# Performance work log

Measured on AMD Instinct MI355X. Metric: run time of the kernel, lower is better.

Reference implementation:

```python
import jax, jax.numpy as jnp
import numpy as np


def setup_inputs() -> dict:
    key = jax.random.key(0)
    kq, kk, kv = jax.random.split(key, 3)
    B, S, D = 16, 2048, 128
    q = jax.random.normal(kq, (B, S, D), dtype=jnp.float32)
    k = jax.random.normal(kk, (B, S, D), dtype=jnp.float32)
    v = jax.random.normal(kv, (B, S, D), dtype=jnp.float32)
    return {"q": q, "k": k, "v": v}


def reference(q, k, v):
    # q: (B, Sq, Dk), k: (B, Skv, Dk), v: (B, Skv, Dv)
    d_k = k.shape[-1]
    scale = 1.0 / jnp.sqrt(jnp.asarray(d_k, dtype=q.dtype))
    scores = jnp.einsum("bqd,bkd->bqk", q, k) * scale  # (B, Sq, Skv)
    # causal mask: strictly-upper-triangular positions set to -inf (mask=True in init)
    Sq = q.shape[-2]
    causal = jnp.triu(jnp.ones((Sq, Sq), dtype=bool), k=1)
    scores = jnp.where(causal, -jnp.inf, scores)
    attn = jax.nn.softmax(scores, axis=-1)
    return jnp.einsum("bqk,bkd->bqd", attn, v)
```

## Files before the change

kernel.cpp:

```cpp
#include <hip/hip_runtime.h>
#include <hip/hip_bf16.h>

typedef __bf16 bf16;
typedef bf16 bf16x8 __attribute__((ext_vector_type(8)));
typedef bf16 bf16x4 __attribute__((ext_vector_type(4)));
typedef float f32x4 __attribute__((ext_vector_type(4)));

#define DHEAD 128
#define SCL2 0.1275500811965365f
#define NINF (-__builtin_inff())

__device__ __forceinline__ unsigned pk2(float a, float b) {
  bf16 x = (bf16)a, y = (bf16)b;
  unsigned short ux = __builtin_bit_cast(unsigned short, x);
  unsigned short uy = __builtin_bit_cast(unsigned short, y);
  return ((unsigned)uy << 16) | (unsigned)ux;
}

#define ACC_FLOATS (1024 * 64 * 128)
#define ML_OFF ACC_FLOATS
#define WS_NEED ((size_t)(ACC_FLOATS + 1024 * 64 * 2) * 4)

__global__ __launch_bounds__(256) void fa_split(
    const float* __restrict__ Q, const float* __restrict__ K,
    const float* __restrict__ V, float* __restrict__ ws, int S)
{
  const int bid  = blockIdx.x;
  const int r    = bid >> 8;
  const int i    = bid & 255;
  const int b    = i & 15;
  const int idx  = i >> 4;
  const int qt   = (r < 2) ? (31 - idx) : idx;
  const int half = r & 1;
  const int blk  = bid;

  const int t0 = half * (qt + 1);
  const int t1 = t0 + (qt + 1);

  const int tid  = threadIdx.x;
  const int wave = tid >> 6;
  const int lane = tid & 63;
  const int lr   = lane & 15;
  const int lg   = lane >> 4;

  __shared__ bf16 Ks[2][32][136];
  __shared__ bf16 Vt[2][DHEAD][40];
  __shared__ bf16 Ps[4][16][40];

  const size_t bo = (size_t)b * S * DHEAD;
  const float* Qb = Q + bo + (size_t)qt * 64 * DHEAD;
  const float* Kb = K + bo;
  const float* Vb = V + bo;
  const int wrow0 = qt * 64 + wave * 16;

  const int j   = tid & 31;
  const int prw = tid >> 5;
  const int d4  = j << 2;
  const int Gw  = (j >> 1) & 3;

  bf16x8 qf[4];
  {
    const float* qr = Qb + (size_t)(wave * 16 + lr) * DHEAD;
    #pragma unroll
    for (int c = 0; c < 4; ++c) {
      const float4 u0 = *reinterpret_cast<const float4*>(qr + c * 32 + lg * 8);
      const float4 u1 = *reinterpret_cast<const float4*>(qr + c * 32 + lg * 8 + 4);
      bf16x8 f;
      f[0] = (bf16)u0.x; f[1] = (bf16)u0.y; f[2] = (bf16)u0.z; f[3] = (bf16)u0.w;
      f[4] = (bf16)u1.x; f[5] = (bf16)u1.y; f[6] = (bf16)u1.z; f[7] = (bf16)u1.w;
      qf[c] = f;
    }
  }

  f32x4 oacc[8];
  #pragma unroll
  for (int ii = 0; ii < 8; ++ii) oacc[ii] = (f32x4){0.f, 0.f, 0.f, 0.f};
  float m = NINF, l = 0.f;

  float4 kA[2], kB[2], vA[2], vB[2];
  auto load_tile = [&](int kc) {
    #pragma unroll
    for (int ps = 0; ps < 2; ++ps) {
      const int kv = kc + 2 * (prw + 8 * ps);
      const float* kp = Kb + (size_t)kv * DHEAD + d4;
      const float* vp = Vb + (size_t)kv * DHEAD + d4;
      kA[ps] = *reinterpret_cast<const float4*>(kp);
      kB[ps] = *reinterpret_cast<const float4*>(kp + DHEAD);
      vA[ps] = *reinterpret_cast<const float4*>(vp);
      vB[ps] = *reinterpret_cast<const float4*>(vp + DHEAD);
    }
  };
  auto write_tile = [&](int buf) {
    #pragma unroll
    for (int ps = 0; ps < 2; ++ps) {
      const int kvp = prw + 8 * ps;
      bf16x4 ka, kb;
      ka[0] = (bf16)kA[ps].x; ka[1] = (bf16)kA[ps].y;
      ka[2] = (bf16)kA[ps].z; ka[3] = (bf16)kA[ps].w;
      kb[0] = (bf16)kB[ps].x; kb[1] = (bf16)kB[ps].y;
      kb[2] = (bf16)kB[ps].z; kb[3] = (bf16)kB[ps].w;
      *reinterpret_cast<bf16x4*>(&Ks[buf][2 * kvp][d4])     = ka;
      *reinterpret_cast<bf16x4*>(&Ks[buf][2 * kvp + 1][d4]) = kb;
      const int pS = kvp ^ (Gw << 2);
      const float* fa = &vA[ps].x;
      const float* fb = &vB[ps].x;
      #pragma unroll
      for (int c = 0; c < 4; ++c) {
        *reinterpret_cast<unsigned*>(&Vt[buf][d4 + c][2 * pS]) = pk2(fa[c], fb[c]);
      }
    }
  };

  load_tile(t0 * 32);
  write_tile(0);
  if (t0 + 1 < t1) load_tile((t0 + 1) * 32);

  int cur = 0;
  for (int t = t0; t < t1; ++t) {
    __syncthreads();
    if (t + 1 < t1) write_tile(cur ^ 1);
    if (t + 2 < t1) load_tile((t + 2) * 32);

    const int kc = t * 32;
    if (kc <= wrow0 + 15) {
      f32x4 s0 = {0.f, 0.f, 0.f, 0.f}, s1 = {0.f, 0.f, 0.f, 0.f};
      __builtin_amdgcn_s_setprio(1);
      #pragma unroll
      for (int c = 0; c < 4; ++c) {
        const bf16x8 kf0 = *reinterpret_cast<const bf16x8*>(&Ks[cur][lr][c * 32 + lg * 8]);
        const bf16x8 kf1 = *reinterpret_cast<const bf16x8*>(&Ks[cur][16 + lr][c * 32 + lg * 8]);
        s0 = __builtin_amdgcn_mfma_f32_16x16x32_bf16(kf0, qf[c], s0, 0, 0, 0);
        s1 = __builtin_amdgcn_mfma_f32_16x16x32_bf16(kf1, qf[c], s1, 0, 0, 0);
      }
      __builtin_amdgcn_s_setprio(0);

      const int qg = wrow0 + lr;
      float x0[4], x1[4];
      if (kc + 31 > wrow0) {
        #pragma unroll
        for (int rr = 0; rr < 4; ++rr) {
          x0[rr] = (kc + 4 * lg + rr      > qg) ? NINF : s0[rr] * SCL2;
          x1[rr] = (kc + 16 + 4 * lg + rr > qg) ? NINF : s1[rr] * SCL2;
        }
      } else {
        #pragma unroll
        for (int rr = 0; rr < 4; ++rr) { x0[rr] = s0[rr] * SCL2; x1[rr] = s1[rr] * SCL2; }
      }
      float tm = NINF;
      #pragma unroll
      for (int rr = 0; rr < 4; ++rr) tm = fmaxf(tm, fmaxf(x0[rr], x1[rr]));
      tm = fmaxf(tm, __shfl_xor(tm, 16));
      tm = fmaxf(tm, __shfl_xor(tm, 32));

      if (!__all(tm <= m + 8.0f)) {
        const float mn = fmaxf(m, tm);
        const float al = __builtin_exp2f(m - mn);
        m = mn; l *= al;
        #pragma unroll
        for (int rr = 0; rr < 4; ++rr) {
          const float ar = __shfl(al, 4 * lg + rr);
          #pragma unroll
          for (int ds = 0; ds < 8; ++ds) oacc[ds][rr] *= ar;
        }
      }

      float p0[4], p1[4];
      float ts = 0.f;
      #pragma unroll
      for (int rr = 0; rr < 4; ++rr) {
        p0[rr] = __builtin_exp2f(x0[rr] - m);
        p1[rr] = __builtin_exp2f(x1[rr] - m);
        ts += p0[rr] + p1[rr];
      }
      ts += __shfl_xor(ts, 16);
      ts += __shfl_xor(ts, 32);
      l += ts;

      *reinterpret_cast<unsigned*>(&Ps[wave][lr][4 * lg])          = pk2(p0[0], p0[1]);
      *reinterpret_cast<unsigned*>(&Ps[wave][lr][4 * lg + 2])      = pk2(p0[2], p0[3]);
      *reinterpret_cast<unsigned*>(&Ps[wave][lr][16 + 4 * lg])     = pk2(p1[0], p1[1]);
      *reinterpret_cast<unsigned*>(&Ps[wave][lr][16 + 4 * lg + 2]) = pk2(p1[2], p1[3]);

      const bf16x8 pf = *reinterpret_cast<const bf16x8*>(&Ps[wave][lr][lg * 8]);
      __builtin_amdgcn_s_setprio(1);
      #pragma unroll
      for (int ds = 0; ds < 8; ++ds) {
        const int G = (2 * ds + (lr >> 3)) & 3;
        const bf16x8 vf = *reinterpret_cast<const bf16x8*>(&Vt[cur][ds * 16 + lr][8 * (lg ^ G)]);
        oacc[ds] = __builtin_amdgcn_mfma_f32_16x16x32_bf16(pf, vf, oacc[ds], 0, 0, 0);
      }
      __builtin_amdgcn_s_setprio(0);
    }
    cur ^= 1;
  }

  float* aw = ws + (size_t)blk * 8192 + (size_t)(wave * 16) * 128;
  #pragma unroll
  for (int rr = 0; rr < 4; ++rr) {
    #pragma unroll
    for (int ds = 0; ds < 8; ++ds) {
      aw[(4 * lg + rr) * 128 + ds * 16 + lr] = oacc[ds][rr];
    }
  }
  if (lg == 0) {
    float* mlp = ws + ML_OFF + (size_t)(blk * 64 + wave * 16 + lr) * 2;
    mlp[0] = m;
    mlp[1] = l;
  }
}

__global__ __launch_bounds__(256) void fa_merge(
    const float* __restrict__ ws, float* __restrict__ O, int S)
{
  const int blk2 = blockIdx.x;
  const int b  = blk2 >> 5;
  const int qt = blk2 & 31;
  const int tid = threadIdx.x;
  const int row = tid >> 2;
  const int c0  = (tid & 3) * 32;

  const int idx  = (qt >= 16) ? (31 - qt) : qt;
  const int base = (qt >= 16) ? 0 : 512;
  const int blk0 = base + (idx << 4) + b;
  const int blk1 = blk0 + 256;

  const float* ml0 = ws + ML_OFF + (size_t)(blk0 * 64 + row) * 2;
  const float* ml1 = ws + ML_OFF + (size_t)(blk1 * 64 + row) * 2;
  const float m0 = ml0[0], l0 = ml0[1];
  const float m1 = ml1[0], l1 = ml1[1];
  const float mm = fmaxf(m0, m1);
  const float a0 = __builtin_exp2f(m0 - mm);
  const float a1 = __builtin_exp2f(m1 - mm);
  const float inv = 1.0f / (a0 * l0 + a1 * l1);

  const float* w0 = ws + (size_t)blk0 * 8192 + (size_t)row * 128 + c0;
  const float* w1 = ws + (size_t)blk1 * 8192 + (size_t)row * 128 + c0;
  float* out = O + ((size_t)b * S + qt * 64 + row) * DHEAD + c0;

  #pragma unroll
  for (int qd = 0; qd < 8; ++qd) {
    const float4 u0 = *reinterpret_cast<const float4*>(w0 + qd * 4);
    const float4 u1 = *reinterpret_cast<const float4*>(w1 + qd * 4);
    float4 o;
    o.x = (a0 * u0.x + a1 * u1.x) * inv;
    o.y = (a0 * u0.y + a1 * u1.y) * inv;
    o.z = (a0 * u0.z + a1 * u1.z) * inv;
    o.w = (a0 * u0.w + a1 * u1.w) * inv;
    *reinterpret_cast<float4*>(out + qd * 4) = o;
  }
}

__global__ __launch_bounds__(256) void fa_fwd(
    const float* __restrict__ Q, const float* __restrict__ K,
    const float* __restrict__ V, float* __restrict__ O, int S)
{
  const int bid = blockIdx.x;
  const int prb = bid & 255;
  const int hb  = bid >> 8;
  const int b   = prb & 15;
  const int jj  = prb >> 4;
  const int qt  = hb ? jj : (31 - jj);

  const int tid  = threadIdx.x;
  const int wave = tid >> 6;
  const int lane = tid & 63;
  const int lr   = lane & 15;
  const int lg   = lane >> 4;

  __shared__ bf16 Ks[2][32][136];
  __shared__ bf16 Vt[2][DHEAD][40];
  __shared__ bf16 Ps[4][16][40];

  const size_t bo = (size_t)b * S * DHEAD;
  const float* Qb = Q + bo + (size_t)qt * 64 * DHEAD;
  const float* Kb = K + bo;
  const float* Vb = V + bo;
  const int wrow0 = qt * 64 + wave * 16;

  const int j   = tid & 31;
  const int prw = tid >> 5;
  const int d4  = j << 2;
  const int Gw  = (j >> 1) & 3;

  bf16x8 qf[4];
  {
    const float* qr = Qb + (size_t)(wave * 16 + lr) * DHEAD;
    #pragma unroll
    for (int c = 0; c < 4; ++c) {
      const float4 u0 = *reinterpret_cast<const float4*>(qr + c * 32 + lg * 8);
      const float4 u1 = *reinterpret_cast<const float4*>(qr + c * 32 + lg * 8 + 4);
      bf16x8 f;
      f[0] = (bf16)u0.x; f[1] = (bf16)u0.y; f[2] = (bf16)u0.z; f[3] = (bf16)u0.w;
      f[4] = (bf16)u1.x; f[5] = (bf16)u1.y; f[6] = (bf16)u1.z; f[7] = (bf16)u1.w;
      qf[c] = f;
    }
  }

  f32x4 oacc[8];
  #pragma unroll
  for (int ii = 0; ii < 8; ++ii) oacc[ii] = (f32x4){0.f, 0.f, 0.f, 0.f};
  float m = NINF, l = 0.f;

  const int nt = 2 * (qt + 1);
  float4 kA[2], kB[2], vA[2], vB[2];

  auto load_tile = [&](int kc) {
    #pragma unroll
    for (int ps = 0; ps < 2; ++ps) {
      const int kv = kc + 2 * (prw + 8 * ps);
      const float* kp = Kb + (size_t)kv * DHEAD + d4;
      const float* vp = Vb + (size_t)kv * DHEAD + d4;
      kA[ps] = *reinterpret_cast<const float4*>(kp);
      kB[ps] = *reinterpret_cast<const float4*>(kp + DHEAD);
      vA[ps] = *reinterpret_cast<const float4*>(vp);
      vB[ps] = *reinterpret_cast<const float4*>(vp + DHEAD);
    }
  };
  auto write_tile = [&](int buf) {
    #pragma unroll
    for (int ps = 0; ps < 2; ++ps) {
      const int kvp = prw + 8 * ps;
      bf16x4 ka, kb;
      ka[0] = (bf16)kA[ps].x; ka[1] = (bf16)kA[ps].y;
      ka[2] = (bf16)kA[ps].z; ka[3] = (bf16)kA[ps].w;
      kb[0] = (bf16)kB[ps].x; kb[1] = (bf16)kB[ps].y;
      kb[2] = (bf16)kB[ps].z; kb[3] = (bf16)kB[ps].w;
      *reinterpret_cast<bf16x4*>(&Ks[buf][2 * kvp][d4])     = ka;
      *reinterpret_cast<bf16x4*>(&Ks[buf][2 * kvp + 1][d4]) = kb;
      const int pS = kvp ^ (Gw << 2);
      const float* fa = &vA[ps].x;
      const float* fb = &vB[ps].x;
      #pragma unroll
      for (int c = 0; c < 4; ++c) {
        *reinterpret_cast<unsigned*>(&Vt[buf][d4 + c][2 * pS]) = pk2(fa[c], fb[c]);
      }
    }
  };

  load_tile(0);
  write_tile(0);
  if (nt > 1) load_tile(32);

  int cur = 0;
  for (int t = 0; t < nt; ++t) {
    __syncthreads();
    if (t + 1 < nt) write_tile(cur ^ 1);
    if (t + 2 < nt) load_tile((t + 2) * 32);

    const int kc = t * 32;
    if (kc <= wrow0 + 15) {
      f32x4 s0 = {0.f, 0.f, 0.f, 0.f}, s1 = {0.f, 0.f, 0.f, 0.f};
      __builtin_amdgcn_s_setprio(1);
      #pragma unroll
      for (int c = 0; c < 4; ++c) {
        const bf16x8 kf0 = *reinterpret_cast<const bf16x8*>(&Ks[cur][lr][c * 32 + lg * 8]);
        const bf16x8 kf1 = *reinterpret_cast<const bf16x8*>(&Ks[cur][16 + lr][c * 32 + lg * 8]);
        s0 = __builtin_amdgcn_mfma_f32_16x16x32_bf16(kf0, qf[c], s0, 0, 0, 0);
        s1 = __builtin_amdgcn_mfma_f32_16x16x32_bf16(kf1, qf[c], s1, 0, 0, 0);
      }
      __builtin_amdgcn_s_setprio(0);

      const int qg = wrow0 + lr;
      float x0[4], x1[4];
      if (kc + 31 > wrow0) {
        #pragma unroll
        for (int rr = 0; rr < 4; ++rr) {
          x0[rr] = (kc + 4 * lg + rr      > qg) ? NINF : s0[rr] * SCL2;
          x1[rr] = (kc + 16 + 4 * lg + rr > qg) ? NINF : s1[rr] * SCL2;
        }
      } else {
        #pragma unroll
        for (int rr = 0; rr < 4; ++rr) { x0[rr] = s0[rr] * SCL2; x1[rr] = s1[rr] * SCL2; }
      }
      float tm = NINF;
      #pragma unroll
      for (int rr = 0; rr < 4; ++rr) tm = fmaxf(tm, fmaxf(x0[rr], x1[rr]));
      tm = fmaxf(tm, __shfl_xor(tm, 16));
      tm = fmaxf(tm, __shfl_xor(tm, 32));

      if (!__all(tm <= m + 8.0f)) {
        const float mn = fmaxf(m, tm);
        const float al = __builtin_exp2f(m - mn);
        m = mn; l *= al;
        #pragma unroll
        for (int rr = 0; rr < 4; ++rr) {
          const float ar = __shfl(al, 4 * lg + rr);
          #pragma unroll
          for (int ds = 0; ds < 8; ++ds) oacc[ds][rr] *= ar;
        }
      }

      float p0[4], p1[4];
      float ts = 0.f;
      #pragma unroll
      for (int rr = 0; rr < 4; ++rr) {
        p0[rr] = __builtin_exp2f(x0[rr] - m);
        p1[rr] = __builtin_exp2f(x1[rr] - m);
        ts += p0[rr] + p1[rr];
      }
      ts += __shfl_xor(ts, 16);
      ts += __shfl_xor(ts, 32);
      l += ts;

      *reinterpret_cast<unsigned*>(&Ps[wave][lr][4 * lg])          = pk2(p0[0], p0[1]);
      *reinterpret_cast<unsigned*>(&Ps[wave][lr][4 * lg + 2])      = pk2(p0[2], p0[3]);
      *reinterpret_cast<unsigned*>(&Ps[wave][lr][16 + 4 * lg])     = pk2(p1[0], p1[1]);
      *reinterpret_cast<unsigned*>(&Ps[wave][lr][16 + 4 * lg + 2]) = pk2(p1[2], p1[3]);

      const bf16x8 pf = *reinterpret_cast<const bf16x8*>(&Ps[wave][lr][lg * 8]);
      __builtin_amdgcn_s_setprio(1);
      #pragma unroll
      for (int ds = 0; ds < 8; ++ds) {
        const int G = (2 * ds + (lr >> 3)) & 3;
        const bf16x8 vf = *reinterpret_cast<const bf16x8*>(&Vt[cur][ds * 16 + lr][8 * (lg ^ G)]);
        oacc[ds] = __builtin_amdgcn_mfma_f32_16x16x32_bf16(pf, vf, oacc[ds], 0, 0, 0);
      }
      __builtin_amdgcn_s_setprio(0);
    }
    cur ^= 1;
  }

  const float linv = 1.0f / l;
  float* Ob = O + bo + (size_t)(qt * 64 + wave * 16) * DHEAD;
  #pragma unroll
  for (int rr = 0; rr < 4; ++rr) {
    const float ir = __shfl(linv, 4 * lg + rr);
    #pragma unroll
    for (int ds = 0; ds < 8; ++ds) {
      Ob[(size_t)(4 * lg + rr) * DHEAD + ds * 16 + lr] = oacc[ds][rr] * ir;
    }
  }
}

extern "C" void kernel_launch(void* const* d_in, const int* in_sizes, int n_in,
                              void* d_out, int out_size, void* d_ws, size_t ws_size,
                              hipStream_t stream) {
  const float* q = (const float*)d_in[0];
  const float* k = (const float*)d_in[1];
  const float* v = (const float*)d_in[2];
  float* o = (float*)d_out;

  const int B = 16;
  const int S = in_sizes[0] / (B * DHEAD);

  if (ws_size >= WS_NEED && S == 2048) {
    float* ws = (float*)d_ws;
    fa_split<<<dim3(1024), dim3(256), 0, stream>>>(q, k, v, ws, S);
    fa_merge<<<dim3(512), dim3(256), 0, stream>>>(ws, o, S);
  } else {
    fa_fwd<<<dim3(512), dim3(256), 0, stream>>>(q, k, v, o, S);
  }
}
```

Measured before the change: 161.1 us.

## Split causal attention KV range four ways per query tile with merge kernel

Adds a four-way split-KV flash attention path. Every query tile's causal key range is divided into four equal chunks, and each chunk runs in its own block (2048 blocks), replacing the earlier two-way split that paired tiles for balance. A merge kernel then combines the four partials using their saved max and sum values. The aim is more parallelism and better load balance across the GPU's compute units, at the cost of twice the workspace traffic for partial outputs plus extra merge work.

```diff
diff --git a/kernel.cpp b/kernel.cpp
--- a/kernel.cpp
+++ b/kernel.cpp
@@ -20,6 +20,237 @@
 #define ACC_FLOATS (1024 * 64 * 128)
 #define ML_OFF ACC_FLOATS
 #define WS_NEED ((size_t)(ACC_FLOATS + 1024 * 64 * 2) * 4)
+
+#define ACC4_FLOATS (2048 * 64 * 128)
+#define ML4_OFF ACC4_FLOATS
+#define WS_NEED4 ((size_t)(ACC4_FLOATS + 2048 * 64 * 2) * 4)
+
+__global__ __launch_bounds__(256) void fa_split4(
+    const float* __restrict__ Q, const float* __restrict__ K,
+    const float* __restrict__ V, float* __restrict__ ws, int S)
+{
+  const int bid  = blockIdx.x;
+  const int half = bid >> 9;
+  const int w    = bid & 511;
+  const int qt   = 31 - (w >> 4);
+  const int b    = w & 15;
+  const int blk  = bid;
+
+  const int NT = 2 * (qt + 1);
+  const int t0 = (half * NT) >> 2;
+  const int t1 = ((half + 1) * NT) >> 2;
+
+  const int tid  = threadIdx.x;
+  const int wave = tid >> 6;
+  const int lane = tid & 63;
+  const int lr   = lane & 15;
+  const int lg   = lane >> 4;
+
+  __shared__ bf16 Ks[32][136];
+  __shared__ bf16 Vt[DHEAD][40];
+  __shared__ bf16 Ps[4][16][40];
+
+  const size_t bo = (size_t)b * S * DHEAD;
+  const float* Qb = Q + bo + (size_t)qt * 64 * DHEAD;
+  const float* Kb = K + bo;
+  const float* Vb = V + bo;
+  const int wrow0 = qt * 64 + wave * 16;
+
+  const int j   = tid & 31;
+  const int prw = tid >> 5;
+  const int d4  = j << 2;
+  const int Gw  = (j >> 1) & 3;
+
+  bf16x8 qf[4];
+  {
+    const float* qr = Qb + (size_t)(wave * 16 + lr) * DHEAD;
+    #pragma unroll
+    for (int c = 0; c < 4; ++c) {
+      const float4 u0 = *reinterpret_cast<const float4*>(qr + c * 32 + lg * 8);
+      const float4 u1 = *reinterpret_cast<const float4*>(qr + c * 32 + lg * 8 + 4);
+      bf16x8 f;
+      f[0] = (bf16)(u0.x * SCL2); f[1] = (bf16)(u0.y * SCL2);
+      f[2] = (bf16)(u0.z * SCL2); f[3] = (bf16)(u0.w * SCL2);
+      f[4] = (bf16)(u1.x * SCL2); f[5] = (bf16)(u1.y * SCL2);
+      f[6] = (bf16)(u1.z * SCL2); f[7] = (bf16)(u1.w * SCL2);
+      qf[c] = f;
+    }
+  }
+
+  f32x4 oacc[8];
+  #pragma unroll
+  for (int ii = 0; ii < 8; ++ii) oacc[ii] = (f32x4){0.f, 0.f, 0.f, 0.f};
+  float m = NINF, l = 0.f;
+
+  float4 kA[2], kB[2], vA[2], vB[2];
+  auto load_tile = [&](int kc) {
+    #pragma unroll
+    for (int ps = 0; ps < 2; ++ps) {
+      const int kv = kc + 2 * (prw + 8 * ps);
+      const float* kp = Kb + (size_t)kv * DHEAD + d4;
+      const float* vp = Vb + (size_t)kv * DHEAD + d4;
+      kA[ps] = *reinterpret_cast<const float4*>(kp);
+      kB[ps] = *reinterpret_cast<const float4*>(kp + DHEAD);
+      vA[ps] = *reinterpret_cast<const float4*>(vp);
+      vB[ps] = *reinterpret_cast<const float4*>(vp + DHEAD);
+    }
+  };
+  auto write_tile = [&]() {
+    #pragma unroll
+    for (int ps = 0; ps < 2; ++ps) {
+      const int kvp = prw + 8 * ps;
+      bf16x4 ka, kb;
+      ka[0] = (bf16)kA[ps].x; ka[1] = (bf16)kA[ps].y;
+      ka[2] = (bf16)kA[ps].z; ka[3] = (bf16)kA[ps].w;
+      kb[0] = (bf16)kB[ps].x; kb[1] = (bf16)kB[ps].y;
+      kb[2] = (bf16)kB[ps].z; kb[3] = (bf16)kB[ps].w;
+      *reinterpret_cast<bf16x4*>(&Ks[2 * kvp][d4])     = ka;
+      *reinterpret_cast<bf16x4*>(&Ks[2 * kvp + 1][d4]) = kb;
+      const int pS = kvp ^ (Gw << 2);
+      const float* fa = &vA[ps].x;
+      const float* fb = &vB[ps].x;
+      #pragma unroll
+      for (int c = 0; c < 4; ++c) {
+        *reinterpret_cast<unsigned*>(&Vt[d4 + c][2 * pS]) = pk2(fa[c], fb[c]);
+      }
+    }
+  };
+
+  if (t0 < t1) load_tile(t0 * 32);
+
+  for (int t = t0; t < t1; ++t) {
+    __syncthreads();
+    write_tile();
+    if (t + 1 < t1) load_tile((t + 1) * 32);
+    __syncthreads();
+
+    const int kc = t * 32;
+    if (kc <= wrow0 + 15) {
+      f32x4 s0 = {0.f, 0.f, 0.f, 0.f}, s1 = {0.f, 0.f, 0.f, 0.f};
+      __builtin_amdgcn_s_setprio(1);
+      #pragma unroll
+      for (int c = 0; c < 4; ++c) {
+        const bf16x8 kf0 = *reinterpret_cast<const bf16x8*>(&Ks[lr][c * 32 + lg * 8]);
+        const bf16x8 kf1 = *reinterpret_cast<const bf16x8*>(&Ks[16 + lr][c * 32 + lg * 8]);
+        s0 = __builtin_amdgcn_mfma_f32_16x16x32_bf16(kf0, qf[c], s0, 0, 0, 0);
+        s1 = __builtin_amdgcn_mfma_f32_16x16x32_bf16(kf1, qf[c], s1, 0, 0, 0);
+      }
+      __builtin_amdgcn_s_setprio(0);
+
+      const int qg = wrow0 + lr;
+      float x0[4], x1[4];
+      if (kc + 31 > wrow0) {
+        #pragma unroll
+        for (int rr = 0; rr < 4; ++rr) {
+          x0[rr] = (kc + 4 * lg + rr      > qg) ? NINF : s0[rr];
+          x1[rr] = (kc + 16 + 4 * lg + rr > qg) ? NINF : s1[rr];
+        }
+      } else {
+        #pragma unroll
+        for (int rr = 0; rr < 4; ++rr) { x0[rr] = s0[rr]; x1[rr] = s1[rr]; }
+      }
+      float tm = NINF;
+      #pragma unroll
+      for (int rr = 0; rr < 4; ++rr) tm = fmaxf(tm, fmaxf(x0[rr], x1[rr]));
+      tm = fmaxf(tm, __shfl_xor(tm, 16));
+      tm = fmaxf(tm, __shfl_xor(tm, 32));
+
+      if (!__all(tm <= m + 8.0f)) {
+        const float mn = fmaxf(m, tm);
+        const float al = __builtin_exp2f(m - mn);
+        m = mn; l *= al;
+        #pragma unroll
+        for (int rr = 0; rr < 4; ++rr) {
+          const float ar = __shfl(al, 4 * lg + rr);
+          #pragma unroll
+          for (int ds = 0; ds < 8; ++ds) oacc[ds][rr] *= ar;
+        }
+      }
+
+      float p0[4], p1[4];
+      float ts = 0.f;
+      #pragma unroll
+      for (int rr = 0; rr < 4; ++rr) {
+        p0[rr] = __builtin_exp2f(x0[rr] - m);
+        p1[rr] = __builtin_exp2f(x1[rr] - m);
+        ts += p0[rr] + p1[rr];
+      }
+      ts += __shfl_xor(ts, 16);
+      ts += __shfl_xor(ts, 32);
+      l += ts;
+
+      *reinterpret_cast<unsigned*>(&Ps[wave][lr][4 * lg])          = pk2(p0[0], p0[1]);
+      *reinterpret_cast<unsigned*>(&Ps[wave][lr][4 * lg + 2])      = pk2(p0[2], p0[3]);
+      *reinterpret_cast<unsigned*>(&Ps[wave][lr][16 + 4 * lg])     = pk2(p1[0], p1[1]);
+      *reinterpret_cast<unsigned*>(&Ps[wave][lr][16 + 4 * lg + 2]) = pk2(p1[2], p1[3]);
+
+      const bf16x8 pf = *reinterpret_cast<const bf16x8*>(&Ps[wave][lr][lg * 8]);
+      __builtin_amdgcn_s_setprio(1);
+      #pragma unroll
+      for (int ds = 0; ds < 8; ++ds) {
+        const int G = (2 * ds + (lr >> 3)) & 3;
+        const bf16x8 vf = *reinterpret_cast<const bf16x8*>(&Vt[ds * 16 + lr][8 * (lg ^ G)]);
+        oacc[ds] = __builtin_amdgcn_mfma_f32_16x16x32_bf16(pf, vf, oacc[ds], 0, 0, 0);
+      }
+      __builtin_amdgcn_s_setprio(0);
+    }
+  }
+
+  float* aw = ws + (size_t)blk * 8192 + (size_t)(wave * 16) * 128;
+  #pragma unroll
+  for (int rr = 0; rr < 4; ++rr) {
+    #pragma unroll
+    for (int ds = 0; ds < 8; ++ds) {
+      aw[(4 * lg + rr) * 128 + ds * 16 + lr] = oacc[ds][rr];
+    }
+  }
+  if (lg == 0) {
+    float* mlp = ws + ML4_OFF + (size_t)(blk * 64 + wave * 16 + lr) * 2;
+    mlp[0] = m;
+    mlp[1] = l;
+  }
+}
+
+__global__ __launch_bounds__(256) void fa_merge4(
+    const float* __restrict__ ws, float* __restrict__ O, int S)
+{
+  const int blk2 = blockIdx.x;
+  const int b  = blk2 >> 5;
+  const int qt = blk2 & 31;
+  const int tid = threadIdx.x;
+  const int row = tid >> 2;
+  const int c0  = (tid & 3) * 32;
+
+  const int w = (31 - qt) * 16 + b;
+  float mi[4], li[4];
+  float mm = NINF;
+  #pragma unroll
+  for (int i = 0; i < 4; ++i) {
+    const float* ml = ws + ML4_OFF + (size_t)((i * 512 + w) * 64 + row) * 2;
+    mi[i] = ml[0]; li[i] = ml[1];
+    mm = fmaxf(mm, mi[i]);
+  }
+  float a[4], den = 0.f;
+  #pragma unroll
+  for (int i = 0; i < 4; ++i) { a[i] = __builtin_exp2f(mi[i] - mm); den += a[i] * li[i]; }
+  const float inv = 1.0f / den;
+
+  float* out = O + ((size_t)b * S + qt * 64 + row) * DHEAD + c0;
+  #pragma unroll
+  for (int qd = 0; qd < 8; ++qd) {
+    float4 acc = {0.f, 0.f, 0.f, 0.f};
+    #pragma unroll
+    for (int i = 0; i < 4; ++i) {
+      const float* wp = ws + (size_t)(i * 512 + w) * 8192 + (size_t)row * 128 + c0;
+      const float4 u = *reinterpret_cast<const float4*>(wp + qd * 4);
+      acc.x += a[i] * u.x; acc.y += a[i] * u.y;
+      acc.z += a[i] * u.z; acc.w += a[i] * u.w;
+    }
+    float4 o;
+    o.x = acc.x * inv; o.y = acc.y * inv; o.z = acc.z * inv; o.w = acc.w * inv;
+    *reinterpret_cast<float4*>(out + qd * 4) = o;
+  }
+}
 
 __global__ __launch_bounds__(256) void fa_split(
     const float* __restrict__ Q, const float* __restrict__ K,
@@ -443,7 +674,11 @@
   const int B = 16;
   const int S = in_sizes[0] / (B * DHEAD);
 
-  if (ws_size >= WS_NEED && S == 2048) {
+  if (ws_size >= WS_NEED4 && S == 2048) {
+    float* ws = (float*)d_ws;
+    fa_split4<<<dim3(2048), dim3(256), 0, stream>>>(q, k, v, ws, S);
+    fa_merge4<<<dim3(512), dim3(256), 0, stream>>>(ws, o, S);
+  } else if (ws_size >= WS_NEED && S == 2048) {
     float* ws = (float*)d_ws;
     fa_split<<<dim3(1024), dim3(256), 0, stream>>>(q, k, v, ws, S);
     fa_merge<<<dim3(512), dim3(256), 0, stream>>>(ws, o, S);
```

Measured after the change: 185.4 us. +15.1%, slower.
